# Optimization experiments

Hardware: AMD Instinct MI355X
Metric: run time of the kernel (lower is better)

The kernel has to match this reference:

```python
import jax, jax.numpy as jnp
import numpy as np

B, S, H, L, NH, OUT = 64, 512, 512, 2, 8, 1
HD = H // NH
SKIP_INTERVAL = 2
EPS = 1e-5


def ln(x, g, b):
    m = x.mean(-1, keepdims=True)
    v = x.var(-1, keepdims=True)
    return (x - m) / jnp.sqrt(v + EPS) * g + b


def setup_inputs() -> dict:
    key = jax.random.key(0)
    ks = iter(jax.random.split(key, 64))
    def nrm(shape, s=0.02):
        return jax.random.normal(next(ks), shape, jnp.float32) * s
    inp = {
        'x': jax.random.normal(next(ks), (B, S, H), jnp.float32),
        # stacked per-layer LSTM params (input_size == hidden_size == H)
        'Wi': nrm((L, 4 * H, H)), 'bi': jnp.zeros((L, 4 * H), jnp.float32).at[:, H:2 * H].set(1.0),
        'Wh': nrm((L, 4 * H, H)), 'bh': jnp.zeros((L, 4 * H), jnp.float32).at[:, H:2 * H].set(1.0),
        'g_in': jnp.ones((L, 4 * H), jnp.float32), 'b_in': jnp.zeros((L, 4 * H), jnp.float32),
        'g_hid': jnp.ones((L, 4 * H), jnp.float32), 'b_hid': jnp.zeros((L, 4 * H), jnp.float32),
        'g_cell': jnp.ones((L, H), jnp.float32), 'b_cell': jnp.zeros((L, H), jnp.float32),
        # highway per layer
        'hw_Wt': nrm((L, H, H)), 'hw_bt': jnp.zeros((L, H), jnp.float32),
        'hw_Wc': nrm((L, H, H)), 'hw_bc': jnp.full((L, H), -1.0, jnp.float32),
        'hw_Wh': nrm((L, H, H)), 'hw_bh': jnp.zeros((L, H), jnp.float32),
        # attention
        'Wq': nrm((H, H)), 'bq': jnp.zeros((H,), jnp.float32),
        'Wk': nrm((H, H)), 'bk': jnp.zeros((H,), jnp.float32),
        'Wv': nrm((H, H)), 'bv': jnp.zeros((H,), jnp.float32),
        'Wo': nrm((H, H)), 'bo': jnp.zeros((H,), jnp.float32),
        'att_g': jnp.ones((H,), jnp.float32), 'att_b': jnp.zeros((H,), jnp.float32),
        # output norm + projection head
        'on_g': jnp.ones((H,), jnp.float32), 'on_b': jnp.zeros((H,), jnp.float32),
        'Wp1': nrm((H // 2, H)), 'bp1': jnp.zeros((H // 2,), jnp.float32),
        'Wp2': nrm((OUT, H // 2)), 'bp2': jnp.zeros((OUT,), jnp.float32),
    }
    return inp


def _forward(x, Wi, bi, Wh, bh, g_in, b_in, g_hid, b_hid, g_cell, b_cell,
             hw_Wt, hw_bt, hw_Wc, hw_bc, hw_Wh, hw_bh,
             Wq, bq, Wk, bk, Wv, bv, Wo, bo, att_g, att_b,
             on_g, on_b, Wp1, bp1, Wp2, bp2):
    def lstm_layer(seq, l):
        # precompute input projection + its LayerNorm for all timesteps: [B,S,4H]
        ip = ln(jnp.einsum('bsh,gh->bsg', seq, Wi[l]) + bi[l], g_in[l], b_in[l])
        def step(carry, ip_t):
            h, c = carry
            hp = ln(h @ Wh[l].T + bh[l], g_hid[l], b_hid[l])
            i_, f_, g_, o_ = jnp.split(ip_t + hp, 4, axis=-1)
            c = jax.nn.sigmoid(f_) * c + jax.nn.sigmoid(i_) * jnp.tanh(g_)
            h = jax.nn.sigmoid(o_) * jnp.tanh(ln(c, g_cell[l], b_cell[l]))
            return (h, c), h
        h0 = jnp.zeros((seq.shape[0], H), seq.dtype)
        _, hs = jax.lax.scan(step, (h0, h0), jnp.swapaxes(ip, 0, 1))
        return jnp.swapaxes(hs, 0, 1)  # [B,S,H]

    seq = x
    for l in range(L):
        h_seq = lstm_layer(seq, l)
        # highway network
        tg = jax.nn.sigmoid(h_seq @ hw_Wt[l].T + hw_bt[l])
        cg = jax.nn.sigmoid(h_seq @ hw_Wc[l].T + hw_bc[l])
        tr = jax.nn.relu(h_seq @ hw_Wh[l].T + hw_bh[l])
        h_seq = tg * tr + cg * h_seq
        # skip connection every SKIP_INTERVAL layers
        if l > 0 and (l + 1) % SKIP_INTERVAL == 0:
            h_seq = h_seq + seq
        seq = h_seq

    # multi-head self-attention with residual + LayerNorm
    def heads(y):
        return jnp.swapaxes(y.reshape(B, S, NH, HD), 1, 2)  # [B,NH,S,HD]
    q = heads(seq @ Wq.T + bq)
    k = heads(seq @ Wk.T + bk)
    v = heads(seq @ Wv.T + bv)
    scale = 1.0 / float(np.sqrt(HD))
    scores = jnp.einsum('bnqd,bnkd->bnqk', q, k) * scale
    aw = jax.nn.softmax(scores, axis=-1)
    ctx = jnp.einsum('bnqk,bnkd->bnqd', aw, v)
    ctx = jnp.swapaxes(ctx, 1, 2).reshape(B, S, H)
    att = ln(ctx @ Wo.T + bo + seq, att_g, att_b)

    # last timestep -> output norm -> MLP head
    last = ln(att[:, -1], on_g, on_b)
    hmid = jax.nn.relu(last @ Wp1.T + bp1)
    return hmid @ Wp2.T + bp2  # [B, OUT]


def reference(x, Wi, bi, Wh, bh, g_in, b_in, g_hid, b_hid, g_cell, b_cell,
              hw_Wt, hw_bt, hw_Wc, hw_bc, hw_Wh, hw_bh,
              Wq, bq, Wk, bk, Wv, bv, Wo, bo, att_g, att_b,
              on_g, on_b, Wp1, bp1, Wp2, bp2):
    return _forward(x, Wi, bi, Wh, bh, g_in, b_in, g_hid, b_hid, g_cell, b_cell,
                    hw_Wt, hw_bt, hw_Wc, hw_bc, hw_Wh, hw_bh,
                    Wq, bq, Wk, bk, Wv, bv, Wo, bo, att_g, att_b,
                    on_g, on_b, Wp1, bp1, Wp2, bp2)
```

## Files before the change

kernel.cpp:

```cpp
#include <hip/hip_runtime.h>

#define EPS_LN 1e-5f

static constexpr int Bn  = 64;
static constexpr int Sn  = 512;
static constexpr int Hn  = 512;
static constexpr int G4n = 2048;

typedef unsigned int uint32;
typedef unsigned long long uint64;
typedef _Float16 h2v __attribute__((ext_vector_type(2)));
typedef _Float16 h8v __attribute__((ext_vector_type(8)));
typedef float f4v __attribute__((ext_vector_type(4)));

__device__ __forceinline__ float sigf(float x)     { return 1.0f / (1.0f + __expf(-x)); }
__device__ __forceinline__ float tanhfast(float x) { return 1.0f - 2.0f / (1.0f + __expf(2.0f * x)); }

__device__ __forceinline__ float dot2h(uint32 w, uint32 h, float acc) {
#if defined(__has_builtin)
#if __has_builtin(__builtin_amdgcn_fdot2)
  return __builtin_amdgcn_fdot2(__builtin_bit_cast(h2v, w), __builtin_bit_cast(h2v, h), acc, false);
#define DOT2_DONE 1
#endif
#endif
#ifndef DOT2_DONE
  h2v wv = __builtin_bit_cast(h2v, w);
  h2v hv = __builtin_bit_cast(h2v, h);
  return acc + (float)wv.x * (float)hv.x + (float)wv.y * (float)hv.y;
#endif
}
__device__ __forceinline__ uint32 packh2(float a, float b) {
  h2v v; v.x = (_Float16)a; v.y = (_Float16)b;
  return __builtin_bit_cast(uint32, v);
}

__device__ __forceinline__ float blk_sum(float v, float* sm, int tid) {
#pragma unroll
  for (int o = 32; o; o >>= 1) v += __shfl_down(v, o, 64);
  __syncthreads();
  if ((tid & 63) == 0) sm[tid >> 6] = v;
  __syncthreads();
  return sm[0] + sm[1] + sm[2] + sm[3];
}
__device__ __forceinline__ float blk_max(float v, float* sm, int tid) {
#pragma unroll
  for (int o = 32; o; o >>= 1) v = fmaxf(v, __shfl_down(v, o, 64));
  __syncthreads();
  if ((tid & 63) == 0) sm[tid >> 6] = v;
  __syncthreads();
  return fmaxf(fmaxf(sm[0], sm[1]), fmaxf(sm[2], sm[3]));
}

__device__ __forceinline__ void blk_sum4_w8(float& a, float& b, float& c, float& d,
                                            float* sm, int tid) {
#pragma unroll
  for (int o = 32; o; o >>= 1) {
    a += __shfl_down(a, o, 64);
    b += __shfl_down(b, o, 64);
    c += __shfl_down(c, o, 64);
    d += __shfl_down(d, o, 64);
  }
  __syncthreads();
  if ((tid & 63) == 0) {
    float4 v; v.x = a; v.y = b; v.z = c; v.w = d;
    *(float4*)&sm[(tid >> 6) * 4] = v;
  }
  __syncthreads();
  float ra = 0.f, rb = 0.f, rc = 0.f, rd = 0.f;
#pragma unroll
  for (int w = 0; w < 8; ++w) {
    float4 v = *(const float4*)&sm[w * 4];
    ra += v.x; rb += v.y; rc += v.z; rd += v.w;
  }
  a = ra; b = rb; c = rc; d = rd;
}

__global__ __launch_bounds__(256) void wh_pack_k(
    const float* __restrict__ Wh, uint32* __restrict__ WhP)
{
  __shared__ float tile[32][33];
  const int l = blockIdx.z;
  const int k0 = blockIdx.x * 32;
  const int n0 = blockIdx.y * 32;
  const int row = threadIdx.x >> 5, col = threadIdx.x & 31;
  const float* src = Wh + (long)l * G4n * Hn;
  uint32* dst = WhP + (long)l * 256 * G4n;
#pragma unroll
  for (int rr = 0; rr < 4; ++rr) {
    int nn = row + rr * 8;
    tile[nn][col] = src[(long)(n0 + nn) * Hn + k0 + col];
  }
  __syncthreads();
#pragma unroll
  for (int rr = 0; rr < 2; ++rr) {
    int kpl = row + rr * 8;
    int kp = (k0 >> 1) + kpl;
    dst[(long)kp * G4n + n0 + col] = packh2(tile[col][2*kpl], tile[col][2*kpl+1]);
  }
}

__global__ void init_zbuf_k(uint64* zbuf)
{
  long i = (long)blockIdx.x * 512 + threadIdx.x;
  zbuf[i] = 0ULL;
}

__global__ __launch_bounds__(256) void gemm_ip_k(
    const float* __restrict__ A,
    const float* __restrict__ Bw,
    const float* __restrict__ bias,
    uint32* __restrict__ C,
    int s0)
{
  __shared__ __align__(16) uint32 Ast[128 * 20];
  __shared__ __align__(16) uint32 Bst[128 * 20];
  const int tid = threadIdx.x;
  const long m0 = (long)blockIdx.y * 128;
  const int n0 = blockIdx.x * 128;

  const int rt = tid >> 1;
  const int hf = tid & 1;
  const long r  = m0 + rt;
  const long b  = r & 63;
  const long sl = r >> 6;
  const float* Arow = A + (b * Sn + s0 + sl) * Hn + hf * 16;
  const float* Brow = Bw + (long)(n0 + rt) * 512 + hf * 16;
  const int sbase = rt * 20 + hf * 8;

  const int w  = tid >> 6;
  const int l  = tid & 63;
  const int lr = l & 15;
  const int lk = (l >> 4) * 4;

  f4v acc[8][2];
#pragma unroll
  for (int ct = 0; ct < 8; ++ct)
#pragma unroll
    for (int mt = 0; mt < 2; ++mt) {
      acc[ct][mt][0] = 0.f; acc[ct][mt][1] = 0.f;
      acc[ct][mt][2] = 0.f; acc[ct][mt][3] = 0.f;
    }

  float4 pa0 = *(const float4*)(Arow + 0);
  float4 pa1 = *(const float4*)(Arow + 4);
  float4 pa2 = *(const float4*)(Arow + 8);
  float4 pa3 = *(const float4*)(Arow + 12);
  float4 pb0 = *(const float4*)(Brow + 0);
  float4 pb1 = *(const float4*)(Brow + 4);
  float4 pb2 = *(const float4*)(Brow + 8);
  float4 pb3 = *(const float4*)(Brow + 12);

  for (int ks = 0; ks < 16; ++ks) {
    __syncthreads();
    {
      uint4 ua0, ua1, ub0, ub1;
      ua0.x = packh2(pa0.x, pa0.y); ua0.y = packh2(pa0.z, pa0.w);
      ua0.z = packh2(pa1.x, pa1.y); ua0.w = packh2(pa1.z, pa1.w);
      ua1.x = packh2(pa2.x, pa2.y); ua1.y = packh2(pa2.z, pa2.w);
      ua1.z = packh2(pa3.x, pa3.y); ua1.w = packh2(pa3.z, pa3.w);
      ub0.x = packh2(pb0.x, pb0.y); ub0.y = packh2(pb0.z, pb0.w);
      ub0.z = packh2(pb1.x, pb1.y); ub0.w = packh2(pb1.z, pb1.w);
      ub1.x = packh2(pb2.x, pb2.y); ub1.y = packh2(pb2.z, pb2.w);
      ub1.z = packh2(pb3.x, pb3.y); ub1.w = packh2(pb3.z, pb3.w);
      *(uint4*)&Ast[sbase]     = ua0;
      *(uint4*)&Ast[sbase + 4] = ua1;
      *(uint4*)&Bst[sbase]     = ub0;
      *(uint4*)&Bst[sbase + 4] = ub1;
    }
    __syncthreads();
    if (ks + 1 < 16) {
      const int ko = (ks + 1) * 32;
      pa0 = *(const float4*)(Arow + ko + 0);
      pa1 = *(const float4*)(Arow + ko + 4);
      pa2 = *(const float4*)(Arow + ko + 8);
      pa3 = *(const float4*)(Arow + ko + 12);
      pb0 = *(const float4*)(Brow + ko + 0);
      pb1 = *(const float4*)(Brow + ko + 4);
      pb2 = *(const float4*)(Brow + ko + 8);
      pb3 = *(const float4*)(Brow + ko + 12);
    }
    uint4 aw0 = *(const uint4*)&Ast[(w*32 + lr) * 20 + lk];
    uint4 aw1 = *(const uint4*)&Ast[(w*32 + 16 + lr) * 20 + lk];
    h8v af0 = __builtin_bit_cast(h8v, aw0);
    h8v af1 = __builtin_bit_cast(h8v, aw1);
#pragma unroll
    for (int ct = 0; ct < 8; ++ct) {
      uint4 bw4 = *(const uint4*)&Bst[(ct*16 + lr) * 20 + lk];
      h8v bf = __builtin_bit_cast(h8v, bw4);
      acc[ct][0] = __builtin_amdgcn_mfma_f32_16x16x32_f16(af0, bf, acc[ct][0], 0, 0, 0);
      acc[ct][1] = __builtin_amdgcn_mfma_f32_16x16x32_f16(af1, bf, acc[ct][1], 0, 0, 0);
    }
  }

  float bs[8];
#pragma unroll
  for (int ct = 0; ct < 8; ++ct) bs[ct] = bias[n0 + ct*16 + lr];
  const long mbase = m0 + w*32 + (l >> 4) * 4;
#pragma unroll
  for (int ct = 0; ct < 8; ++ct) {
    const int cp = (n0 + ct*16 + lr) >> 1;
#pragma unroll
    for (int mt = 0; mt < 2; ++mt) {
#pragma unroll
      for (int j = 0; j < 4; ++j) {
        float v = acc[ct][mt][j] + bs[ct];
        float vh = __shfl_xor(v, 1, 64);
        if (!(l & 1)) {
          const long m = mbase + mt*16 + j;
          C[m * 1024 + cp] = packh2(v, vh);
        }
      }
    }
  }
}

__global__ __launch_bounds__(256) void ipstats_k(
    const uint32* __restrict__ X, float* __restrict__ st)
{
  const long row = blockIdx.x;
  const uint32* xr = X + row * 1024;
  const int tid = threadIdx.x;
  __shared__ float sm[4];
  uint4 w = *(const uint4*)(xr + tid*4);
  h2v a = __builtin_bit_cast(h2v, w.x);
  h2v b = __builtin_bit_cast(h2v, w.y);
  h2v c = __builtin_bit_cast(h2v, w.z);
  h2v d = __builtin_bit_cast(h2v, w.w);
  float v[8] = {(float)a.x,(float)a.y,(float)b.x,(float)b.y,
                (float)c.x,(float)c.y,(float)d.x,(float)d.y};
  float s1 = 0.f, s2 = 0.f;
#pragma unroll
  for (int i = 0; i < 8; ++i) { s1 += v[i]; s2 += v[i]*v[i]; }
  s1 = blk_sum(s1, sm, tid);
  s2 = blk_sum(s2, sm, tid);
  if (tid == 0) {
    const float mean = s1 * (1.f/2048.f);
    const float rstd = rsqrtf(s2 * (1.f/2048.f) - mean*mean + EPS_LN);
    st[row*2]     = mean;
    st[row*2 + 1] = rstd;
  }
}

__global__ __launch_bounds__(256) void hw_fused_k(
    const float* __restrict__ A,
    const float* __restrict__ Wt, const float* __restrict__ bt,
    const float* __restrict__ Wc, const float* __restrict__ bc,
    const float* __restrict__ Wh3, const float* __restrict__ bh3,
    float* __restrict__ seqout,
    int skip)
{
  __shared__ __align__(16) uint32 Ast[128 * 20];
  __shared__ __align__(16) uint32 Bst[3 * 64 * 20];
  const int tid = threadIdx.x;
  const long m0 = (long)blockIdx.y * 128;
  const int n0 = blockIdx.x * 64;

  const int rt = tid >> 1;
  const int hf = tid & 1;
  const float* Arow = A + (m0 + rt) * 512 + hf * 16;
  const int sbaseA = rt * 20 + hf * 8;

  const int u1 = tid;
  const int u2 = tid + 256;
  const int m1_ = u1 >> 7, r1_ = (u1 >> 1) & 63, h1_ = u1 & 1;
  const int m2_ = u2 >> 7, r2_ = (u2 >> 1) & 63, h2_ = u2 & 1;
  const float* bsrc1 = (m1_ == 0 ? Wt : (m1_ == 1 ? Wc : Wh3)) + (long)(n0 + r1_) * 512 + h1_ * 16;
  const float* bsrc2 = (m2_ == 0 ? Wt : (m2_ == 1 ? Wc : Wh3)) + (long)(n0 + r2_) * 512 + h2_ * 16;
  const int sbaseB1 = m1_ * 1280 + r1_ * 20 + h1_ * 8;
  const int sbaseB2 = m2_ * 1280 + r2_ * 20 + h2_ * 8;

  const int w  = tid >> 6;
  const int l  = tid & 63;
  const int lr = l & 15;
  const int lk = (l >> 4) * 4;

  f4v acc[3][4][2];
#pragma unroll
  for (int mat = 0; mat < 3; ++mat)
#pragma unroll
    for (int nt = 0; nt < 4; ++nt)
#pragma unroll
      for (int mt = 0; mt < 2; ++mt) {
        acc[mat][nt][mt][0] = 0.f; acc[mat][nt][mt][1] = 0.f;
        acc[mat][nt][mt][2] = 0.f; acc[mat][nt][mt][3] = 0.f;
      }

  for (int ks = 0; ks < 16; ++ks) {
    const int ko = ks * 32;
    __syncthreads();
    {
      float4 a0 = *(const float4*)(Arow + ko + 0);
      float4 a1 = *(const float4*)(Arow + ko + 4);
      float4 a2 = *(const float4*)(Arow + ko + 8);
      float4 a3 = *(const float4*)(Arow + ko + 12);
      uint4 ua0, ua1;
      ua0.x = packh2(a0.x, a0.y); ua0.y = packh2(a0.z, a0.w);
      ua0.z = packh2(a1.x, a1.y); ua0.w = packh2(a1.z, a1.w);
      ua1.x = packh2(a2.x, a2.y); ua1.y = packh2(a2.z, a2.w);
      ua1.z = packh2(a3.x, a3.y); ua1.w = packh2(a3.z, a3.w);
      *(uint4*)&Ast[sbaseA]     = ua0;
      *(uint4*)&Ast[sbaseA + 4] = ua1;
    }
    {
      float4 b0 = *(const float4*)(bsrc1 + ko + 0);
      float4 b1 = *(const float4*)(bsrc1 + ko + 4);
      float4 b2 = *(const float4*)(bsrc1 + ko + 8);
      float4 b3 = *(const float4*)(bsrc1 + ko + 12);
      uint4 ub0, ub1;
      ub0.x = packh2(b0.x, b0.y); ub0.y = packh2(b0.z, b0.w);
      ub0.z = packh2(b1.x, b1.y); ub0.w = packh2(b1.z, b1.w);
      ub1.x = packh2(b2.x, b2.y); ub1.y = packh2(b2.z, b2.w);
      ub1.z = packh2(b3.x, b3.y); ub1.w = packh2(b3.z, b3.w);
      *(uint4*)&Bst[sbaseB1]     = ub0;
      *(uint4*)&Bst[sbaseB1 + 4] = ub1;
    }
    if (tid < 128) {
      float4 b0 = *(const float4*)(bsrc2 + ko + 0);
      float4 b1 = *(const float4*)(bsrc2 + ko + 4);
      float4 b2 = *(const float4*)(bsrc2 + ko + 8);
      float4 b3 = *(const float4*)(bsrc2 + ko + 12);
      uint4 ub0, ub1;
      ub0.x = packh2(b0.x, b0.y); ub0.y = packh2(b0.z, b0.w);
      ub0.z = packh2(b1.x, b1.y); ub0.w = packh2(b1.z, b1.w);
      ub1.x = packh2(b2.x, b2.y); ub1.y = packh2(b2.z, b2.w);
      ub1.z = packh2(b3.x, b3.y); ub1.w = packh2(b3.z, b3.w);
      *(uint4*)&Bst[sbaseB2]     = ub0;
      *(uint4*)&Bst[sbaseB2 + 4] = ub1;
    }
    __syncthreads();

    uint4 aw0 = *(const uint4*)&Ast[(w*32 + lr) * 20 + lk];
    uint4 aw1 = *(const uint4*)&Ast[(w*32 + 16 + lr) * 20 + lk];
    h8v af0 = __builtin_bit_cast(h8v, aw0);
    h8v af1 = __builtin_bit_cast(h8v, aw1);
#pragma unroll
    for (int mat = 0; mat < 3; ++mat) {
#pragma unroll
      for (int nt = 0; nt < 4; ++nt) {
        uint4 bw4 = *(const uint4*)&Bst[mat*1280 + (nt*16 + lr) * 20 + lk];
        h8v bf = __builtin_bit_cast(h8v, bw4);
        acc[mat][nt][0] = __builtin_amdgcn_mfma_f32_16x16x32_f16(af0, bf, acc[mat][nt][0], 0, 0, 0);
        acc[mat][nt][1] = __builtin_amdgcn_mfma_f32_16x16x32_f16(af1, bf, acc[mat][nt][1], 0, 0, 0);
      }
    }
  }

  float bsT[4], bsC[4], bsH[4];
#pragma unroll
  for (int nt = 0; nt < 4; ++nt) {
    const int col = n0 + nt*16 + lr;
    bsT[nt] = bt[col];
    bsC[nt] = bc[col];
    bsH[nt] = bh3[col];
  }
  const long mbase = m0 + w*32 + (l >> 4) * 4;
#pragma unroll
  for (int nt = 0; nt < 4; ++nt) {
    const int col = n0 + nt*16 + lr;
#pragma unroll
    for (int mt = 0; mt < 2; ++mt) {
#pragma unroll
      for (int j = 0; j < 4; ++j) {
        const long m = mbase + mt*16 + j;
        const float t1 = acc[0][nt][mt][j] + bsT[nt];
        const float t2 = acc[1][nt][mt][j] + bsC[nt];
        const float t3 = acc[2][nt][mt][j] + bsH[nt];
        const float hvv = A[m * 512 + col];
        const float svv = skip ? seqout[m * 512 + col] : 0.f;
        seqout[m * 512 + col] = sigf(t1) * fmaxf(t3, 0.f) + sigf(t2) * hvv + svv;
      }
    }
  }
}

__global__ __launch_bounds__(256) void gemm_m64_k(
    const float* __restrict__ A, long lda,
    const float* __restrict__ Bw,
    const float* __restrict__ bias,
    float* __restrict__ P,
    int N, int K)
{
  __shared__ float As[64][64];
  __shared__ float Bs[64][64];
  const int tid = threadIdx.x;
  const int n0 = blockIdx.x * 64;
  const int kc = blockIdx.y;
  const int Kc = K / gridDim.y;
  const int tx = tid & 15, ty = tid >> 4;
  const int row = tid >> 2, q = tid & 3;
  float acc[4][4];
#pragma unroll
  for (int i = 0; i < 4; ++i)
#pragma unroll
    for (int j = 0; j < 4; ++j) acc[i][j] = 0.f;

  for (int k0 = kc * Kc; k0 < kc * Kc + Kc; k0 += 64) {
    float4 a[4], b[4];
#pragma unroll
    for (int c = 0; c < 4; ++c) {
      a[c] = *(const float4*)(A  + (long)row * lda       + k0 + q*16 + c*4);
      b[c] = *(const float4*)(Bw + (long)(n0 + row) * K  + k0 + q*16 + c*4);
    }
    __syncthreads();
#pragma unroll
    for (int c = 0; c < 4; ++c) {
      int kb = q*16 + c*4;
      As[kb+0][row]=a[c].x; As[kb+1][row]=a[c].y; As[kb+2][row]=a[c].z; As[kb+3][row]=a[c].w;
      Bs[kb+0][row]=b[c].x; Bs[kb+1][row]=b[c].y; Bs[kb+2][row]=b[c].z; Bs[kb+3][row]=b[c].w;
    }
    __syncthreads();
#pragma unroll
    for (int kk = 0; kk < 64; ++kk) {
      float4 av = *(const float4*)&As[kk][ty*4];
      float4 bv = *(const float4*)&Bs[kk][tx*4];
      float am[4] = {av.x, av.y, av.z, av.w};
      float bm[4] = {bv.x, bv.y, bv.z, bv.w};
#pragma unroll
      for (int i = 0; i < 4; ++i)
#pragma unroll
        for (int j = 0; j < 4; ++j) acc[i][j] += am[i] * bm[j];
    }
  }
#pragma unroll
  for (int i = 0; i < 4; ++i) {
    int m = ty*4 + i;
    float* pr = P + ((long)kc * 64 + m) * N + n0 + tx*4;
#pragma unroll
    for (int j = 0; j < 4; ++j) {
      float bb = bias ? bias[n0 + tx*4 + j] : 0.f;
      pr[j] = acc[i][j] + bb;
    }
  }
}

__global__ __launch_bounds__(512, 2) void lstm_seqz_k(
    const uint32* __restrict__ WhP,
    const float* __restrict__ bh,
    const uint32* __restrict__ ipc,
    const float* __restrict__ ipstats,
    const float* __restrict__ g_in, const float* __restrict__ b_in,
    const float* __restrict__ g_hid, const float* __restrict__ b_hid,
    const float* __restrict__ g_cell, const float* __restrict__ b_cell,
    float* __restrict__ hst, float* __restrict__ cst,
    float* __restrict__ hseq,
    uint64* __restrict__ zbuf,
    int t0, int nsteps, int gbase)
{
  const int blk = blockIdx.x;
  const int g   = blk & 31;
  const int kq  = blk >> 5;
  const int tid = threadIdx.x;
  const int b0  = g*2, b1 = g*2 + 1;
  const int r   = tid >> 1;
  const int kh  = tid & 1;
  __shared__ __align__(16) uint32 hp0[264];
  __shared__ __align__(16) uint32 hp1[264];
  __shared__ float sm[32];

  uint4 wreg[32];
  {
    const uint32* base = WhP + (long)(kh * 128) * 2048 + (kq*256 + r);
#pragma unroll
    for (int i = 0; i < 32; ++i) {
      wreg[i].x = base[(long)(4*i + 0) * 2048];
      wreg[i].y = base[(long)(4*i + 1) * 2048];
      wreg[i].z = base[(long)(4*i + 2) * 2048];
      wreg[i].w = base[(long)(4*i + 3) * 2048];
    }
  }

  float bhr[4], ghr[4], bhir[4], ginr[4], binr[4];
#pragma unroll
  for (int q = 0; q < 4; ++q) {
    bhr[q]  = bh[q*512 + tid];
    ghr[q]  = g_hid[q*512 + tid];
    bhir[q] = b_hid[q*512 + tid];
    ginr[q] = g_in[q*512 + tid];
    binr[q] = b_in[q*512 + tid];
  }
  const float gcv = g_cell[tid];
  const float bcv = b_cell[tid];
  float c0 = cst[b0*512 + tid];
  float c1 = cst[b1*512 + tid];
  float h0 = hst[b0*512 + tid];
  float h1 = hst[b1*512 + tid];

  {
    const float p0 = __shfl_xor(h0, 1, 64);
    const float p1 = __shfl_xor(h1, 1, 64);
    if (!(tid & 1)) {
      const int j = tid >> 1;
      const int jj = (j < 128) ? j : j + 4;
      hp0[jj] = packh2(h0, p0);
      hp1[jj] = packh2(h1, p1);
    }
  }
  __syncthreads();

  const long myword = (long)(kq*256 + r) * 2 + kh;
  const uint32* hb0 = hp0 + kh * 132;
  const uint32* hb1 = hp1 + kh * 132;

  for (int ts = 0; ts < nsteps; ++ts) {
    const int gstep = gbase + ts;
    const uint32 tagw = (uint32)gstep;
    uint64* zp = zbuf + (long)(gstep & 1) * 131072 + (long)g * 4096;

    const uint32* iprow0 = ipc + ((long)ts * 64 + b0) * 1024 + (tid >> 1);
    const uint32* iprow1 = ipc + ((long)ts * 64 + b1) * 1024 + (tid >> 1);
    const float2 st0 = *(const float2*)(ipstats + ((long)ts * 64 + b0) * 2);
    const float2 st1 = *(const float2*)(ipstats + ((long)ts * 64 + b1) * 2);
    float ip0[4], ip1[4];
#pragma unroll
    for (int q = 0; q < 4; ++q) {
      h2v v0 = __builtin_bit_cast(h2v, iprow0[q*256]);
      h2v v1 = __builtin_bit_cast(h2v, iprow1[q*256]);
      const float r0 = kh ? (float)v0.y : (float)v0.x;
      const float r1 = kh ? (float)v1.y : (float)v1.x;
      ip0[q] = (r0 - st0.x) * st0.y * ginr[q] + binr[q];
      ip1[q] = (r1 - st1.x) * st1.y * ginr[q] + binr[q];
    }

    float a0 = 0.f, a1 = 0.f;
#pragma unroll
    for (int i = 0; i < 32; ++i) {
      const uint4 w  = wreg[i];
      const uint4 hv0 = *(const uint4*)&hb0[4*i];
      const uint4 hv1 = *(const uint4*)&hb1[4*i];
      a0 = dot2h(w.x, hv0.x, a0); a0 = dot2h(w.y, hv0.y, a0);
      a0 = dot2h(w.z, hv0.z, a0); a0 = dot2h(w.w, hv0.w, a0);
      a1 = dot2h(w.x, hv1.x, a1); a1 = dot2h(w.y, hv1.y, a1);
      a1 = dot2h(w.z, hv1.z, a1); a1 = dot2h(w.w, hv1.w, a1);
    }
    a0 += __shfl_xor(a0, 1, 64);
    a1 += __shfl_xor(a1, 1, 64);

    {
      const float zval = kh ? a1 : a0;
      const uint64 w = ((uint64)tagw << 32) | (uint64)__builtin_bit_cast(uint32, zval);
      __hip_atomic_store(zp + myword, w, __ATOMIC_RELAXED, __HIP_MEMORY_SCOPE_AGENT);
    }

    float z0[4], z1[4];
    {
      uint64 v0[4], v1[4];
      int pend = 0xff;
      while (pend) {
#pragma unroll
        for (int q = 0; q < 4; ++q) {
          const long base = (long)(q*512 + tid) * 2;
          if (pend & (1 << q)) {
            uint64 w = __hip_atomic_load(zp + base, __ATOMIC_RELAXED, __HIP_MEMORY_SCOPE_AGENT);
            if ((uint32)(w >> 32) == tagw) { v0[q] = w; pend &= ~(1 << q); }
          }
          if (pend & (16 << q)) {
            uint64 w = __hip_atomic_load(zp + base + 1, __ATOMIC_RELAXED, __HIP_MEMORY_SCOPE_AGENT);
            if ((uint32)(w >> 32) == tagw) { v1[q] = w; pend &= ~(16 << q); }
          }
        }
        if (pend) __builtin_amdgcn_s_sleep(2);
      }
#pragma unroll
      for (int q = 0; q < 4; ++q) {
        z0[q] = __builtin_bit_cast(float, (uint32)v0[q]) + bhr[q];
        z1[q] = __builtin_bit_cast(float, (uint32)v1[q]) + bhr[q];
      }
    }

    float s10 = z0[0]+z0[1]+z0[2]+z0[3];
    float s20 = z0[0]*z0[0] + z0[1]*z0[1] + z0[2]*z0[2] + z0[3]*z0[3];
    float s11 = z1[0]+z1[1]+z1[2]+z1[3];
    float s21 = z1[0]*z1[0] + z1[1]*z1[1] + z1[2]*z1[2] + z1[3]*z1[3];
    blk_sum4_w8(s10, s20, s11, s21, sm, tid);
    const float m0 = s10 * (1.f/2048.f);
    const float r0 = rsqrtf(s20 * (1.f/2048.f) - m0*m0 + EPS_LN);
    const float m1 = s11 * (1.f/2048.f);
    const float r1 = rsqrtf(s21 * (1.f/2048.f) - m1*m1 + EPS_LN);

    const float gi0 = ip0[0] + (z0[0] - m0) * r0 * ghr[0] + bhir[0];
    const float gf0 = ip0[1] + (z0[1] - m0) * r0 * ghr[1] + bhir[1];
    const float gg0 = ip0[2] + (z0[2] - m0) * r0 * ghr[2] + bhir[2];
    const float go0 = ip0[3] + (z0[3] - m0) * r0 * ghr[3] + bhir[3];
    const float gi1 = ip1[0] + (z1[0] - m1) * r1 * ghr[0] + bhir[0];
    const float gf1 = ip1[1] + (z1[1] - m1) * r1 * ghr[1] + bhir[1];
    const float gg1 = ip1[2] + (z1[2] - m1) * r1 * ghr[2] + bhir[2];
    const float go1 = ip1[3] + (z1[3] - m1) * r1 * ghr[3] + bhir[3];

    c0 = sigf(gf0) * c0 + sigf(gi0) * tanhfast(gg0);
    c1 = sigf(gf1) * c1 + sigf(gi1) * tanhfast(gg1);

    float t10 = c0, t20 = c0*c0, t11 = c1, t21 = c1*c1;
    blk_sum4_w8(t10, t20, t11, t21, sm, tid);
    const float n0 = t10 * (1.f/512.f);
    const float q0r = rsqrtf(t20 * (1.f/512.f) - n0*n0 + EPS_LN);
    const float n1 = t11 * (1.f/512.f);
    const float q1r = rsqrtf(t21 * (1.f/512.f) - n1*n1 + EPS_LN);
    h0 = sigf(go0) * tanhfast((c0 - n0) * q0r * gcv + bcv);
    h1 = sigf(go1) * tanhfast((c1 - n1) * q1r * gcv + bcv);

    if (kq == 0) {
      hseq[((long)b0 * Sn + t0 + ts) * Hn + tid] = h0;
      hseq[((long)b1 * Sn + t0 + ts) * Hn + tid] = h1;
    }

    const float p0 = __shfl_xor(h0, 1, 64);
    const float p1 = __shfl_xor(h1, 1, 64);
    if (!(tid & 1)) {
      const int j = tid >> 1;
      const int jj = (j < 128) ? j : j + 4;
      hp0[jj] = packh2(h0, p0);
      hp1[jj] = packh2(h1, p1);
    }
    __syncthreads();
  }
  if (kq == 0) {
    hst[b0*512 + tid] = h0; hst[b1*512 + tid] = h1;
    cst[b0*512 + tid] = c0; cst[b1*512 + tid] = c1;
  }
}

__global__ void init_hc_k(float* h, float* c)
{
  int i = blockIdx.x * 256 + threadIdx.x;
  h[i] = 0.f; c[i] = 0.f;
}

__global__ __launch_bounds__(256) void qkh_k(
    const float* __restrict__ qlst, const float* __restrict__ Wk,
    const float* __restrict__ bk,
    float* __restrict__ qkh, float* __restrict__ qbk)
{
  const int hd = blockIdx.x, cg = blockIdx.y;
  const int b = threadIdx.x & 63, sc = threadIdx.x >> 6;
  const int col0 = cg * 128 + sc * 32;
  float qreg[64];
  const float* qp = qlst + b*512 + hd*64;
#pragma unroll
  for (int j4 = 0; j4 < 16; ++j4) {
    float4 v = *(const float4*)(qp + j4*4);
    qreg[j4*4+0]=v.x; qreg[j4*4+1]=v.y; qreg[j4*4+2]=v.z; qreg[j4*4+3]=v.w;
  }
  float acc[32];
#pragma unroll
  for (int c = 0; c < 32; ++c) acc[c] = 0.f;
  for (int j = 0; j < 64; ++j) {
    float qv = qreg[j];
    const float* wr = Wk + (long)(hd*64 + j)*512 + col0;
#pragma unroll
    for (int c4 = 0; c4 < 8; ++c4) {
      float4 w = *(const float4*)(wr + c4*4);
      acc[c4*4+0] = __builtin_fmaf(qv, w.x, acc[c4*4+0]);
      acc[c4*4+1] = __builtin_fmaf(qv, w.y, acc[c4*4+1]);
      acc[c4*4+2] = __builtin_fmaf(qv, w.z, acc[c4*4+2]);
      acc[c4*4+3] = __builtin_fmaf(qv, w.w, acc[c4*4+3]);
    }
  }
  float* op = qkh + ((long)b*8 + hd)*512 + col0;
#pragma unroll
  for (int c4 = 0; c4 < 8; ++c4) {
    float4 o;
    o.x = acc[c4*4+0]; o.y = acc[c4*4+1]; o.z = acc[c4*4+2]; o.w = acc[c4*4+3];
    *(float4*)(op + c4*4) = o;
  }
  if (cg == 0 && sc == 0) {
    float s = 0.f;
    for (int j = 0; j < 64; ++j) s += qreg[j] * bk[hd*64 + j];
    qbk[b*8 + hd] = s;
  }
}

__global__ __launch_bounds__(256) void attn2_k(
    const float* __restrict__ seq,
    const float* __restrict__ qkh,
    const float* __restrict__ qbk,
    float* __restrict__ u)
{
  const int b = blockIdx.x, hd = blockIdx.y, tid = threadIdx.x;
  __shared__ __align__(16) float qk[512];
  __shared__ float p[512];
  __shared__ float sm[4];
  qk[tid]       = qkh[((long)b*8 + hd)*512 + tid];
  qk[tid + 256] = qkh[((long)b*8 + hd)*512 + tid + 256];
  __syncthreads();
  const float bias = qbk[b*8 + hd];

  float loc[2]; float mx = -3.0e38f;
#pragma unroll
  for (int v = 0; v < 2; ++v) {
    int s = tid + v*256;
    const float4* sr = (const float4*)(seq + ((long)b*512 + s)*512);
    const float4* qv4 = (const float4*)qk;
    float d = 0.f;
    for (int k4 = 0; k4 < 128; ++k4) {
      float4 sv = sr[k4], qv = qv4[k4];
      d += sv.x*qv.x + sv.y*qv.y + sv.z*qv.z + sv.w*qv.w;
    }
    d = (d + bias) * 0.125f;
    loc[v] = d; mx = fmaxf(mx, d);
  }
  const float M = blk_max(mx, sm, tid);
  float sum = 0.f;
#pragma unroll
  for (int v = 0; v < 2; ++v) {
    int s = tid + v*256;
    float e = __expf(loc[v] - M);
    p[s] = e; sum += e;
  }
  const float SM = blk_sum(sum, sm, tid);
  const float inv = 1.f / SM;

  float u0 = 0.f, u1 = 0.f;
  for (int s = 0; s < 512; ++s) {
    float ps = p[s];
    const float* srow = seq + ((long)b*512 + s)*512;
    u0 = __builtin_fmaf(ps, srow[tid], u0);
    u1 = __builtin_fmaf(ps, srow[tid + 256], u1);
  }
  u[((long)b*8 + hd)*512 + tid]       = u0 * inv;
  u[((long)b*8 + hd)*512 + tid + 256] = u1 * inv;
}

__global__ __launch_bounds__(256) void ctxv_k(
    const float* __restrict__ u, const float* __restrict__ Wv,
    const float* __restrict__ bv, float* __restrict__ ctx)
{
  const int b = blockIdx.x, tid = threadIdx.x;
  __shared__ __align__(16) float ul[8*512];
  for (int i = tid; i < 4096; i += 256) ul[i] = u[(long)b*4096 + i];
  __syncthreads();
#pragma unroll
  for (int v = 0; v < 2; ++v) {
    int n = tid + v*256;
    int hd = n >> 6;
    const float4* wr = (const float4*)(Wv + (long)n*512);
    const float4* uv = (const float4*)&ul[hd*512];
    float acc = 0.f;
    for (int k4 = 0; k4 < 128; ++k4) {
      float4 w = wr[k4], x = uv[k4];
      acc += w.x*x.x + w.y*x.y + w.z*x.z + w.w*x.w;
    }
    ctx[b*512 + n] = acc + bv[n];
  }
}

__global__ __launch_bounds__(256) void head_k(
    const float* __restrict__ ctx,
    const float* __restrict__ Wo, const float* __restrict__ bo,
    const float* __restrict__ seq,
    const float* __restrict__ att_g, const float* __restrict__ att_b,
    const float* __restrict__ on_g, const float* __restrict__ on_b,
    const float* __restrict__ Wp1, const float* __restrict__ bp1,
    const float* __restrict__ Wp2, const float* __restrict__ bp2,
    float* __restrict__ out)
{
  const int b = blockIdx.x, tid = threadIdx.x;
  __shared__ __align__(16) float cs[512];
  __shared__ __align__(16) float buf[512];
  __shared__ float sm[4];
  cs[tid]       = ctx[b*512 + tid];
  cs[tid + 256] = ctx[b*512 + tid + 256];
  __syncthreads();

  const float* srow = seq + ((long)b*512 + 511) * 512;
  float o[2];
#pragma unroll
  for (int v = 0; v < 2; ++v) {
    int j = tid + v*256;
    const float4* w4 = (const float4*)(Wo + (long)j * 512);
    const float4* c4 = (const float4*)cs;
    float acc = 0.f;
    for (int kx = 0; kx < 128; ++kx) {
      float4 w = w4[kx], c = c4[kx];
      acc += w.x*c.x + w.y*c.y + w.z*c.z + w.w*c.w;
    }
    o[v] = acc + bo[j] + srow[j];
  }
  float s1 = o[0] + o[1], s2 = o[0]*o[0] + o[1]*o[1];
  s1 = blk_sum(s1, sm, tid); s2 = blk_sum(s2, sm, tid);
  float m1 = s1 * (1.f/512.f);
  float r1 = rsqrtf(s2 * (1.f/512.f) - m1*m1 + EPS_LN);
  float a[2];
#pragma unroll
  for (int v = 0; v < 2; ++v) {
    int j = tid + v*256;
    a[v] = (o[v] - m1) * r1 * att_g[j] + att_b[j];
  }
  s1 = a[0] + a[1]; s2 = a[0]*a[0] + a[1]*a[1];
  s1 = blk_sum(s1, sm, tid); s2 = blk_sum(s2, sm, tid);
  float m2 = s1 * (1.f/512.f);
  float r2 = rsqrtf(s2 * (1.f/512.f) - m2*m2 + EPS_LN);
#pragma unroll
  for (int v = 0; v < 2; ++v) {
    int j = tid + v*256;
    buf[j] = (a[v] - m2) * r2 * on_g[j] + on_b[j];
  }
  __syncthreads();

  const float4* w1 = (const float4*)(Wp1 + (long)tid * 512);
  const float4* b4 = (const float4*)buf;
  float acc = 0.f;
  for (int kx = 0; kx < 128; ++kx) {
    float4 w = w1[kx], c = b4[kx];
    acc += w.x*c.x + w.y*c.y + w.z*c.z + w.w*c.w;
  }
  float mid = fmaxf(acc + bp1[tid], 0.f);
  float contrib = mid * Wp2[tid];
  float tot = blk_sum(contrib, sm, tid);
  if (tid == 0) out[b] = tot + bp2[0];
}

extern "C" void kernel_launch(void* const* d_in, const int* in_sizes, int n_in,
                              void* d_out, int out_size, void* d_ws, size_t ws_size,
                              hipStream_t stream)
{
  const float* x     = (const float*)d_in[0];
  const float* Wi    = (const float*)d_in[1];
  const float* bi    = (const float*)d_in[2];
  const float* Wh    = (const float*)d_in[3];
  const float* bh    = (const float*)d_in[4];
  const float* g_in  = (const float*)d_in[5];
  const float* b_in  = (const float*)d_in[6];
  const float* g_hid = (const float*)d_in[7];
  const float* b_hid = (const float*)d_in[8];
  const float* g_cell= (const float*)d_in[9];
  const float* b_cell= (const float*)d_in[10];
  const float* hwWt  = (const float*)d_in[11];
  const float* hwbt  = (const float*)d_in[12];
  const float* hwWc  = (const float*)d_in[13];
  const float* hwbc  = (const float*)d_in[14];
  const float* hwWh  = (const float*)d_in[15];
  const float* hwbh  = (const float*)d_in[16];
  const float* Wq    = (const float*)d_in[17];
  const float* bq    = (const float*)d_in[18];
  const float* Wk    = (const float*)d_in[19];
  const float* bk    = (const float*)d_in[20];
  const float* Wv    = (const float*)d_in[21];
  const float* bv    = (const float*)d_in[22];
  const float* Wo    = (const float*)d_in[23];
  const float* bo    = (const float*)d_in[24];
  const float* att_g = (const float*)d_in[25];
  const float* att_b = (const float*)d_in[26];
  const float* on_g  = (const float*)d_in[27];
  const float* on_b  = (const float*)d_in[28];
  const float* Wp1   = (const float*)d_in[29];
  const float* bp1   = (const float*)d_in[30];
  const float* Wp2   = (const float*)d_in[31];
  const float* bp2   = (const float*)d_in[32];
  float* out = (float*)d_out;

  const long SEQF = (long)Bn * Sn * Hn;
  const long WHPF = 2L * 256 * G4n;
  const long ZBF  = 2L * 32 * 2048 * 2;
  const long wsF  = (long)(ws_size / 4);

  float* ws   = (float*)d_ws;
  float* seq  = ws;
  float* hseq = seq  + SEQF;
  uint32* WhP = (uint32*)(hseq + SEQF);
  uint64* zbuf = (uint64*)(hseq + SEQF + WHPF);
  float* hst  = hseq + SEQF + WHPF + 2*ZBF;
  float* cst  = hst  + 32768L;
  float* qlst = cst  + 32768L;
  float* ctx  = qlst + 32768L;
  float* qkh  = ctx  + 32768L;
  float* qbk  = qkh  + 262144L;
  float* uat  = qbk  + 1024L;
  float* ipstats = uat + 262144L;
  float* ipcF = ipstats + 65536L;
  uint32* ipc = (uint32*)ipcF;
  const long baseF = (ipcF - ws);

  int TCH = 512;
  while (TCH > 16 && baseF + (long)TCH * 64 * 1024 > wsF) TCH >>= 1;

  wh_pack_k<<<dim3(16, 64, 2), 256, 0, stream>>>(Wh, WhP);
  init_zbuf_k<<<512, 512, 0, stream>>>(zbuf);

  const int NCH = Sn / TCH;
  const int MROWS = TCH * 64;
  const int NMCH = (Bn * Sn) / MROWS;

  for (int l = 0; l < 2; ++l) {
    const float* seqin = (l == 0) ? x : seq;
    init_hc_k<<<128, 256, 0, stream>>>(hst, cst);
    for (int c = 0; c < NCH; ++c) {
      const int s0 = c * TCH;
      gemm_ip_k<<<dim3(16, TCH/2), 256, 0, stream>>>(seqin, Wi + (long)l*G4n*Hn, bi + l*G4n, ipc, s0);
      ipstats_k<<<TCH*64, 256, 0, stream>>>(ipc, ipstats);
      lstm_seqz_k<<<256, 512, 0, stream>>>(WhP + (long)l*256*G4n, bh + l*G4n, ipc, ipstats,
          g_in + l*G4n, b_in + l*G4n,
          g_hid + l*G4n, b_hid + l*G4n, g_cell + l*Hn, b_cell + l*Hn,
          hst, cst, hseq, zbuf, s0, TCH, l*Sn + s0 + 1);
    }
    for (int mc = 0; mc < NMCH; ++mc) {
      const long m0 = (long)mc * MROWS;
      hw_fused_k<<<dim3(8, MROWS/128), 256, 0, stream>>>(
          hseq + m0*512,
          hwWt + (long)l*Hn*Hn, hwbt + l*Hn,
          hwWc + (long)l*Hn*Hn, hwbc + l*Hn,
          hwWh + (long)l*Hn*Hn, hwbh + l*Hn,
          seq + m0*512, (l == 0) ? 0 : 1);
    }
  }

  gemm_m64_k<<<dim3(8, 1), 256, 0, stream>>>(seq + 511L*512, 512L*512, Wq, bq, qlst, 512, 512);
  qkh_k<<<dim3(8, 4), 256, 0, stream>>>(qlst, Wk, bk, qkh, qbk);
  attn2_k<<<dim3(64, 8), 256, 0, stream>>>(seq, qkh, qbk, uat);
  ctxv_k<<<64, 256, 0, stream>>>(uat, Wv, bv, ctx);
  head_k<<<64, 256, 0, stream>>>(ctx, Wo, bo, seq, att_g, att_b, on_g, on_b, Wp1, bp1, Wp2, bp2, out);
}
```

Measured before the change: 7.928 ms.

## Fuse input-projection LN stats into GEMM epilogue and store hidden sequence as fp16

Row sums and sums of squares for the input-projection LayerNorm are now accumulated in the GEMM epilogue with atomics, removing the separate stats kernel; mean and rstd are derived inside the LSTM kernel. The LSTM writes its hidden sequence as packed fp16 pairs, which the highway kernel loads directly without converting. This cuts one launch and re-read of the projection buffer, and halves hidden-sequence memory traffic. The costs are a memset per chunk, atomic contention, and reduced precision in the highway residual.

```diff
diff --git a/kernel.cpp b/kernel.cpp
--- a/kernel.cpp
+++ b/kernel.cpp
@@ -110,6 +110,7 @@
     const float* __restrict__ Bw,
     const float* __restrict__ bias,
     uint32* __restrict__ C,
+    float* __restrict__ st,
     int s0)
 {
   __shared__ __align__(16) uint32 Ast[128 * 20];
@@ -196,6 +197,30 @@
 #pragma unroll
   for (int ct = 0; ct < 8; ++ct) bs[ct] = bias[n0 + ct*16 + lr];
   const long mbase = m0 + w*32 + (l >> 4) * 4;
+
+#pragma unroll
+  for (int mt = 0; mt < 2; ++mt) {
+#pragma unroll
+    for (int j = 0; j < 4; ++j) {
+      float s1 = 0.f, s2 = 0.f;
+#pragma unroll
+      for (int ct = 0; ct < 8; ++ct) {
+        const float v = acc[ct][mt][j] + bs[ct];
+        s1 += v; s2 += v * v;
+      }
+#pragma unroll
+      for (int o = 1; o < 16; o <<= 1) {
+        s1 += __shfl_xor(s1, o, 16);
+        s2 += __shfl_xor(s2, o, 16);
+      }
+      if (lr == 0) {
+        const long m = mbase + mt*16 + j;
+        atomicAdd(&st[m*2],     s1);
+        atomicAdd(&st[m*2 + 1], s2);
+      }
+    }
+  }
+
 #pragma unroll
   for (int ct = 0; ct < 8; ++ct) {
     const int cp = (n0 + ct*16 + lr) >> 1;
@@ -214,35 +239,8 @@
   }
 }
 
-__global__ __launch_bounds__(256) void ipstats_k(
-    const uint32* __restrict__ X, float* __restrict__ st)
-{
-  const long row = blockIdx.x;
-  const uint32* xr = X + row * 1024;
-  const int tid = threadIdx.x;
-  __shared__ float sm[4];
-  uint4 w = *(const uint4*)(xr + tid*4);
-  h2v a = __builtin_bit_cast(h2v, w.x);
-  h2v b = __builtin_bit_cast(h2v, w.y);
-  h2v c = __builtin_bit_cast(h2v, w.z);
-  h2v d = __builtin_bit_cast(h2v, w.w);
-  float v[8] = {(float)a.x,(float)a.y,(float)b.x,(float)b.y,
-                (float)c.x,(float)c.y,(float)d.x,(float)d.y};
-  float s1 = 0.f, s2 = 0.f;
-#pragma unroll
-  for (int i = 0; i < 8; ++i) { s1 += v[i]; s2 += v[i]*v[i]; }
-  s1 = blk_sum(s1, sm, tid);
-  s2 = blk_sum(s2, sm, tid);
-  if (tid == 0) {
-    const float mean = s1 * (1.f/2048.f);
-    const float rstd = rsqrtf(s2 * (1.f/2048.f) - mean*mean + EPS_LN);
-    st[row*2]     = mean;
-    st[row*2 + 1] = rstd;
-  }
-}
-
 __global__ __launch_bounds__(256) void hw_fused_k(
-    const float* __restrict__ A,
+    const uint32* __restrict__ A,
     const float* __restrict__ Wt, const float* __restrict__ bt,
     const float* __restrict__ Wc, const float* __restrict__ bc,
     const float* __restrict__ Wh3, const float* __restrict__ bh3,
@@ -257,7 +255,7 @@
 
   const int rt = tid >> 1;
   const int hf = tid & 1;
-  const float* Arow = A + (m0 + rt) * 512 + hf * 16;
+  const uint32* Arow = A + (m0 + rt) * 256 + hf * 8;
   const int sbaseA = rt * 20 + hf * 8;
 
   const int u1 = tid;
@@ -289,15 +287,8 @@
     const int ko = ks * 32;
     __syncthreads();
     {
-      float4 a0 = *(const float4*)(Arow + ko + 0);
-      float4 a1 = *(const float4*)(Arow + ko + 4);
-      float4 a2 = *(const float4*)(Arow + ko + 8);
-      float4 a3 = *(const float4*)(Arow + ko + 12);
-      uint4 ua0, ua1;
-      ua0.x = packh2(a0.x, a0.y); ua0.y = packh2(a0.z, a0.w);
-      ua0.z = packh2(a1.x, a1.y); ua0.w = packh2(a1.z, a1.w);
-      ua1.x = packh2(a2.x, a2.y); ua1.y = packh2(a2.z, a2.w);
-      ua1.z = packh2(a3.x, a3.y); ua1.w = packh2(a3.z, a3.w);
+      uint4 ua0 = *(const uint4*)(Arow + ks*16);
+      uint4 ua1 = *(const uint4*)(Arow + ks*16 + 4);
       *(uint4*)&Ast[sbaseA]     = ua0;
       *(uint4*)&Ast[sbaseA + 4] = ua1;
     }
@@ -365,7 +356,8 @@
         const float t1 = acc[0][nt][mt][j] + bsT[nt];
         const float t2 = acc[1][nt][mt][j] + bsC[nt];
         const float t3 = acc[2][nt][mt][j] + bsH[nt];
-        const float hvv = A[m * 512 + col];
+        h2v hp = __builtin_bit_cast(h2v, A[m * 256 + (col >> 1)]);
+        const float hvv = (lr & 1) ? (float)hp.y : (float)hp.x;
         const float svv = skip ? seqout[m * 512 + col] : 0.f;
         seqout[m * 512 + col] = sigf(t1) * fmaxf(t3, 0.f) + sigf(t2) * hvv + svv;
       }
@@ -442,7 +434,7 @@
     const float* __restrict__ g_hid, const float* __restrict__ b_hid,
     const float* __restrict__ g_cell, const float* __restrict__ b_cell,
     float* __restrict__ hst, float* __restrict__ cst,
-    float* __restrict__ hseq,
+    uint32* __restrict__ hseqH,
     uint64* __restrict__ zbuf,
     int t0, int nsteps, int gbase)
 {
@@ -510,6 +502,10 @@
     const uint32* iprow1 = ipc + ((long)ts * 64 + b1) * 1024 + (tid >> 1);
     const float2 st0 = *(const float2*)(ipstats + ((long)ts * 64 + b0) * 2);
     const float2 st1 = *(const float2*)(ipstats + ((long)ts * 64 + b1) * 2);
+    const float ipm0 = st0.x * (1.f/2048.f);
+    const float ipr0 = rsqrtf(st0.y * (1.f/2048.f) - ipm0*ipm0 + EPS_LN);
+    const float ipm1 = st1.x * (1.f/2048.f);
+    const float ipr1 = rsqrtf(st1.y * (1.f/2048.f) - ipm1*ipm1 + EPS_LN);
     float ip0[4], ip1[4];
 #pragma unroll
     for (int q = 0; q < 4; ++q) {
@@ -517,8 +513,8 @@
       h2v v1 = __builtin_bit_cast(h2v, iprow1[q*256]);
       const float r0 = kh ? (float)v0.y : (float)v0.x;
       const float r1 = kh ? (float)v1.y : (float)v1.x;
-      ip0[q] = (r0 - st0.x) * st0.y * ginr[q] + binr[q];
-      ip1[q] = (r1 - st1.x) * st1.y * ginr[q] + binr[q];
+      ip0[q] = (r0 - ipm0) * ipr0 * ginr[q] + binr[q];
+      ip1[q] = (r1 - ipm1) * ipr1 * ginr[q] + binr[q];
     }
 
     float a0 = 0.f, a1 = 0.f;
@@ -598,11 +594,6 @@
     h0 = sigf(go0) * tanhfast((c0 - n0) * q0r * gcv + bcv);
     h1 = sigf(go1) * tanhfast((c1 - n1) * q1r * gcv + bcv);
 
-    if (kq == 0) {
-      hseq[((long)b0 * Sn + t0 + ts) * Hn + tid] = h0;
-      hseq[((long)b1 * Sn + t0 + ts) * Hn + tid] = h1;
-    }
-
     const float p0 = __shfl_xor(h0, 1, 64);
     const float p1 = __shfl_xor(h1, 1, 64);
     if (!(tid & 1)) {
@@ -610,6 +601,10 @@
       const int jj = (j < 128) ? j : j + 4;
       hp0[jj] = packh2(h0, p0);
       hp1[jj] = packh2(h1, p1);
+      if (kq == 0) {
+        hseqH[((long)b0 * Sn + t0 + ts) * 256 + j] = packh2(h0, p0);
+        hseqH[((long)b1 * Sn + t0 + ts) * 256 + j] = packh2(h1, p1);
+      }
     }
     __syncthreads();
   }
@@ -848,17 +843,18 @@
   const float* bp2   = (const float*)d_in[32];
   float* out = (float*)d_out;
 
-  const long SEQF = (long)Bn * Sn * Hn;
-  const long WHPF = 2L * 256 * G4n;
-  const long ZBF  = 2L * 32 * 2048 * 2;
-  const long wsF  = (long)(ws_size / 4);
+  const long SEQF  = (long)Bn * Sn * Hn;
+  const long HSEQF = SEQF / 2;
+  const long WHPF  = 2L * 256 * G4n;
+  const long ZBF   = 2L * 32 * 2048 * 2;
+  const long wsF   = (long)(ws_size / 4);
 
   float* ws   = (float*)d_ws;
   float* seq  = ws;
-  float* hseq = seq  + SEQF;
-  uint32* WhP = (uint32*)(hseq + SEQF);
-  uint64* zbuf = (uint64*)(hseq + SEQF + WHPF);
-  float* hst  = hseq + SEQF + WHPF + 2*ZBF;
+  uint32* hseqH = (uint32*)(seq + SEQF);
+  uint32* WhP = (uint32*)(seq + SEQF + HSEQF);
+  uint64* zbuf = (uint64*)(seq + SEQF + HSEQF + WHPF);
+  float* hst  = seq + SEQF + HSEQF + WHPF + 2*ZBF;
   float* cst  = hst  + 32768L;
   float* qlst = cst  + 32768L;
   float* ctx  = qlst + 32768L;
@@ -885,17 +881,17 @@
     init_hc_k<<<128, 256, 0, stream>>>(hst, cst);
     for (int c = 0; c < NCH; ++c) {
       const int s0 = c * TCH;
-      gemm_ip_k<<<dim3(16, TCH/2), 256, 0, stream>>>(seqin, Wi + (long)l*G4n*Hn, bi + l*G4n, ipc, s0);
-      ipstats_k<<<TCH*64, 256, 0, stream>>>(ipc, ipstats);
+      hipMemsetAsync(ipstats, 0, (size_t)TCH * 64 * 2 * sizeof(float), stream);
+      gemm_ip_k<<<dim3(16, TCH/2), 256, 0, stream>>>(seqin, Wi + (long)l*G4n*Hn, bi + l*G4n, ipc, ipstats, s0);
       lstm_seqz_k<<<256, 512, 0, stream>>>(WhP + (long)l*256*G4n, bh + l*G4n, ipc, ipstats,
           g_in + l*G4n, b_in + l*G4n,
           g_hid + l*G4n, b_hid + l*G4n, g_cell + l*Hn, b_cell + l*Hn,
-          hst, cst, hseq, zbuf, s0, TCH, l*Sn + s0 + 1);
+          hst, cst, hseqH, zbuf, s0, TCH, l*Sn + s0 + 1);
     }
     for (int mc = 0; mc < NMCH; ++mc) {
       const long m0 = (long)mc * MROWS;
       hw_fused_k<<<dim3(8, MROWS/128), 256, 0, stream>>>(
-          hseq + m0*512,
+          hseqH + m0*256,
           hwWt + (long)l*Hn*Hn, hwbt + l*Hn,
           hwWc + (long)l*Hn*Hn, hwbc + l*Hn,
           hwWh + (long)l*Hn*Hn, hwbh + l*Hn,
```

New measurement: 7.801 ms. Within noise of the previous version (-1.6%).
